# Kernel tuning notes

Hardware: AMD Instinct MI355X
Metric: run time of the kernel (lower is better)

Reference implementation:

```python
import jax, jax.numpy as jnp
import numpy as np
import math

B, N, SEEDS, DIM, H = 16, 2048, 4, 512, 8
DS = DIM // H
EPS = 1e-5
LOG_2PI = math.log(2.0 * math.pi)


def setup_inputs() -> dict:
    key = jax.random.key(0)
    ks = jax.random.split(key, 12)
    s = 1.0 / math.sqrt(DIM)
    d = {}
    d["X"] = jax.random.normal(ks[0], (B, N, SEEDS, DIM), jnp.float32)
    # seed parameters (kaiming/xavier-ish init)
    d["M"] = jax.random.uniform(ks[1], (1, SEEDS, DIM), jnp.float32, -s, s) * math.sqrt(6.0)
    d["S"] = jax.random.uniform(ks[2], (1, SEEDS, DIM), jnp.float32, -s, s) * math.sqrt(6.0)
    d["p"] = jax.random.uniform(ks[3], (1, SEEDS), jnp.float32, -0.5, 0.5)
    # linear layers (PyTorch Linear: y = x @ W.T + b)
    d["Wk"] = jax.random.uniform(ks[4], (DIM, DIM), jnp.float32, -s, s)
    d["bk"] = jax.random.uniform(ks[5], (DIM,), jnp.float32, -s, s)
    d["Wv"] = jax.random.uniform(ks[6], (DIM, DIM), jnp.float32, -s, s)
    d["bv"] = jax.random.uniform(ks[7], (DIM,), jnp.float32, -s, s)
    d["Wo"] = jax.random.uniform(ks[8], (DIM, DIM), jnp.float32, -s, s)
    d["bo"] = jax.random.uniform(ks[9], (DIM,), jnp.float32, -s, s)
    # batchnorm affine params (init: weight=1, bias=0)
    d["g0"] = jnp.ones((SEEDS * DIM,), jnp.float32)
    d["b0"] = jnp.zeros((SEEDS * DIM,), jnp.float32)
    d["g1"] = jnp.ones((SEEDS * DIM,), jnp.float32)
    d["b1"] = jnp.zeros((SEEDS * DIM,), jnp.float32)
    return d


def _batchnorm(x, g, b):
    # BatchNorm1d in training mode: batch stats (biased variance), eps=1e-5
    m = x.mean(axis=0)
    v = x.var(axis=0)
    return g * (x - m) / jnp.sqrt(v + EPS) + b


def reference(X, M, S, p, Wk, bk, Wv, bv, Wo, bo, g0, b0, g1, b1):
    mu = M[0].reshape(SEEDS, H, DS)                      # [S,H,DS] per-head seeds
    sigma = jax.nn.softplus(S[0]).reshape(SEEDS, H, DS)  # [S,H,DS]
    logp = jnp.log(jax.nn.softmax(p[0], axis=-1))        # [S]

    K = (X @ Wk.T + bk).reshape(B, N, SEEDS, H, DS)
    V = (X @ Wv.T + bv).reshape(B, N, SEEDS, H, DS)

    # GMM log-likelihood scores: sum over per-head feature dim
    diff = K - mu                                        # [B,N,S,H,DS]
    ll = (-0.5 * LOG_2PI - jnp.log(sigma) - 0.5 * diff * diff / (sigma * sigma)).sum(-1)
    ll = ll + logp[:, None]                              # [B,N,S,H]

    A = jax.nn.softmax(ll / math.sqrt(DIM), axis=1)      # softmax over instances n
    O = mu + jnp.einsum('bnsh,bnshd->bshd', A, V)        # [B,S,H,DS]
    O = O.reshape(B, SEEDS, DIM)                         # head-major feature concat

    O = _batchnorm(O.reshape(B, SEEDS * DIM), g0, b0).reshape(B, SEEDS, DIM)
    O = O + jax.nn.relu(O @ Wo.T + bo)
    O = _batchnorm(O.reshape(B, SEEDS * DIM), g1, b1).reshape(B, SEEDS, DIM)
    return O
```

## Files before the change

### kernel.cpp

```cpp
#include <hip/hip_runtime.h>
#include <hip/hip_bf16.h>

typedef __attribute__((ext_vector_type(4))) float f32x4;
typedef __attribute__((ext_vector_type(8))) short bf16x8;

constexpr int NB = 16, NN = 2048, NS = 4, NDIM = 512, NH = 8, NDS = 64;
constexpr float LOG2PI = 1.8378770664093453f;
constexpr float INV_SQRT_DIM = 0.04419417382415922f;

__device__ inline short f2bf(float f) {
  __hip_bfloat16 h = __float2bfloat16(f);
  return *reinterpret_cast<short*>(&h);
}
__device__ inline float bf2f(short b) {
  union { unsigned u; float f; } v;
  v.u = ((unsigned)(unsigned short)b) << 16;
  return v.f;
}

__device__ inline void gld16(const void* g, void* l) {
  __builtin_amdgcn_global_load_lds(
      (const __attribute__((address_space(1))) void*)g,
      (__attribute__((address_space(3))) void*)l, 16, 0, 0);
}

__global__ __launch_bounds__(256) void cvtx_kernel(
    const float* __restrict__ in, short* __restrict__ out, int n8)
{
  const int stride = gridDim.x * blockDim.x;
  for (int i = blockIdx.x * blockDim.x + threadIdx.x; i < n8; i += stride) {
    const float4 a = reinterpret_cast<const float4*>(in)[(size_t)i * 2];
    const float4 b = reinterpret_cast<const float4*>(in)[(size_t)i * 2 + 1];
    bf16x8 o;
    o[0] = f2bf(a.x); o[1] = f2bf(a.y); o[2] = f2bf(a.z); o[3] = f2bf(a.w);
    o[4] = f2bf(b.x); o[5] = f2bf(b.y); o[6] = f2bf(b.z); o[7] = f2bf(b.w);
    *reinterpret_cast<bf16x8*>(&out[(size_t)i * 8]) = o;
  }
}

__global__ __launch_bounds__(256) void prep_kernel(
    const float* __restrict__ Wv, float* __restrict__ WvT,
    const float* __restrict__ Wk, short* __restrict__ Wkb,
    const float* __restrict__ Mp, const float* __restrict__ Sp,
    const float* __restrict__ pp, const float* __restrict__ bkp,
    float4* __restrict__ gmm, float* __restrict__ lp2)
{
  const int blk = blockIdx.x;
  const int tid = threadIdx.x;
  if (blk < 1024) {
    const int idx = blk * 256 + tid;
    const int d = idx & 63;
    const int i = (idx >> 6) & 511;
    const int h = idx >> 15;
    WvT[idx] = Wv[(size_t)(h * 64 + d) * 512 + i];
  } else if (blk < 1152) {
    const int j = (blk - 1024) * 256 + tid;
    const float4 a = reinterpret_cast<const float4*>(Wk)[(size_t)j * 2];
    const float4 b = reinterpret_cast<const float4*>(Wk)[(size_t)j * 2 + 1];
    bf16x8 o;
    o[0] = f2bf(a.x); o[1] = f2bf(a.y); o[2] = f2bf(a.z); o[3] = f2bf(a.w);
    o[4] = f2bf(b.x); o[5] = f2bf(b.y); o[6] = f2bf(b.z); o[7] = f2bf(b.w);
    *reinterpret_cast<bf16x8*>(&Wkb[(size_t)j * 8]) = o;
  } else {
    const int idx = (blk - 1152) * 256 + tid;
    const int Jg = idx & 511;
    const float sv = Sp[idx];
    const float sig = log1pf(expf(sv));
    float4 o;
    o.x = Mp[idx];
    o.y = (-0.5f * LOG2PI - logf(sig)) * INV_SQRT_DIM;
    o.z = (0.5f / (sig * sig)) * INV_SQRT_DIM;
    o.w = bkp[Jg];
    gmm[idx] = o;
    if (idx < 4) {
      const float p0 = pp[0], p1 = pp[1], p2 = pp[2], p3 = pp[3];
      const float pmx = fmaxf(fmaxf(p0, p1), fmaxf(p2, p3));
      const float lse = pmx + logf(expf(p0 - pmx) + expf(p1 - pmx) +
                                   expf(p2 - pmx) + expf(p3 - pmx));
      lp2[idx] = (pp[idx] - lse) * INV_SQRT_DIM;
    }
  }
}

__global__ __launch_bounds__(256) void kproj_kernel(
    const short* __restrict__ Xb, const short* __restrict__ Wkb,
    const float4* __restrict__ gmm, const float* __restrict__ lp2,
    float* __restrict__ ll_ws)
{
  __shared__ short As[2][128 * 64];
  __shared__ short Bs[2][128 * 64];

  const int bid0 = blockIdx.x;
  const int bid = (bid0 & 7) * 512 + (bid0 >> 3);
  const int ct = bid & 3;
  const int mt = bid >> 2;
  const int m0 = mt * 128;
  const int c0 = ct * 128;

  const int t = threadIdx.x;
  const int l = t & 63;
  const int w = t >> 6;
  const int wr = w >> 1, wc = w & 1;
  const int lg = l >> 4, lr = l & 15;

  f32x4 acc[4][4] = {};

  const int g8 = (l & 7) ^ (l >> 3);
  const size_t gxa = (size_t)(m0 + w * 32 + (l >> 3)) * NDIM + g8 * 8;
  const size_t gba = (size_t)(c0 + w * 32 + (l >> 3)) * NDIM + g8 * 8;
  const int dA = (w * 32) * 64;

  auto stage = [&](int buf, int ts) {
    const int k0 = ts << 6;
    #pragma unroll
    for (int q = 0; q < 4; ++q) {
      const size_t so = (size_t)(q * 8) * NDIM + k0;
      const int dd = dA + (q * 8) * 64;
      gld16(&Xb[gxa + so],  (char*)&As[buf][dd]);
      gld16(&Wkb[gba + so], (char*)&Bs[buf][dd]);
    }
  };

  auto compute = [&](int buf) {
    #pragma unroll
    for (int kk = 0; kk < 64; kk += 32) {
      bf16x8 a[4], b[4];
      #pragma unroll
      for (int i = 0; i < 4; ++i) {
        const int r = wr * 64 + i * 16 + lr;
        const int byte = r * 128 + ((((kk >> 3) + lg) ^ (lr & 7)) << 4);
        a[i] = *reinterpret_cast<const bf16x8*>((const char*)&As[buf][0] + byte);
      }
      #pragma unroll
      for (int j = 0; j < 4; ++j) {
        const int r = wc * 64 + j * 16 + lr;
        const int byte = r * 128 + ((((kk >> 3) + lg) ^ (lr & 7)) << 4);
        b[j] = *reinterpret_cast<const bf16x8*>((const char*)&Bs[buf][0] + byte);
      }
      #pragma unroll
      for (int i = 0; i < 4; ++i) {
        #pragma unroll
        for (int j = 0; j < 4; ++j)
          acc[i][j] = __builtin_amdgcn_mfma_f32_16x16x32_bf16(a[i], b[j], acc[i][j], 0, 0, 0);
      }
    }
  };

  stage(0, 0);
  __builtin_amdgcn_sched_barrier(0);
  for (int ts = 0; ts < 7; ++ts) {
    stage((ts + 1) & 1, ts + 1);
    asm volatile("s_waitcnt vmcnt(8)" ::: "memory");
    __builtin_amdgcn_s_barrier();
    compute(ts & 1);
    __builtin_amdgcn_s_barrier();
  }
  asm volatile("s_waitcnt vmcnt(0)" ::: "memory");
  __builtin_amdgcn_s_barrier();
  compute(1);
  __builtin_amdgcn_sched_barrier(0);


  const float l0 = lp2[0], l1 = lp2[1], l2 = lp2[2], l3 = lp2[3];
  const float lpv[4] = {l0, l1, l2, l3};

  float part[4][4];
  #pragma unroll
  for (int i = 0; i < 4; ++i)
    #pragma unroll
    for (int e = 0; e < 4; ++e) part[i][e] = 0.f;

  #pragma unroll
  for (int j = 0; j < 4; ++j) {
    const int Jg = c0 + wc * 64 + j * 16 + lr;
    #pragma unroll
    for (int e = 0; e < 4; ++e) {
      const float4 gw = gmm[e * NDIM + Jg];
      #pragma unroll
      for (int i = 0; i < 4; ++i) {
        const float kv = acc[i][j][e] + gw.w;
        const float d = kv - gw.x;
        part[i][e] += gw.y - d * d * gw.z;
      }
    }
  }
  #pragma unroll
  for (int off = 1; off < 16; off <<= 1) {
    #pragma unroll
    for (int i = 0; i < 4; ++i)
      #pragma unroll
      for (int e = 0; e < 4; ++e)
        part[i][e] += __shfl_xor(part[i][e], off, 64);
  }
  if (lr == 0) {
    const int h = ct * 2 + wc;
    #pragma unroll
    for (int i = 0; i < 4; ++i) {
      #pragma unroll
      for (int e = 0; e < 4; ++e) {
        const int R = m0 + wr * 64 + i * 16 + 4 * lg + e;
        const int bn = R >> 2;
        const int bb = bn >> 11;
        const int nn = bn & (NN - 1);
        ll_ws[((size_t)((bb * NS + e) * NH + h)) * NN + nn] = part[i][e] + lpv[e];
      }
    }
  }
}

__global__ __launch_bounds__(256) void stats_kernel(
    const float* __restrict__ ll_ws, float* __restrict__ mxs,
    float* __restrict__ rsum)
{
  __shared__ float sred[8];
  const int g = blockIdx.x;
  const int t = threadIdx.x;
  const int w = t >> 6, l = t & 63;
  const float* ll = ll_ws + (size_t)g * NN;

  float v8[8];
  float mx = -1e30f;
  #pragma unroll
  for (int i = 0; i < 8; ++i) { v8[i] = ll[t + i * 256]; mx = fmaxf(mx, v8[i]); }
  #pragma unroll
  for (int off = 1; off < 64; off <<= 1) mx = fmaxf(mx, __shfl_xor(mx, off, 64));
  if (l == 0) sred[w] = mx;
  __syncthreads();
  mx = fmaxf(fmaxf(sred[0], sred[1]), fmaxf(sred[2], sred[3]));

  float sum = 0.f;
  #pragma unroll
  for (int i = 0; i < 8; ++i) sum += expf(v8[i] - mx);
  #pragma unroll
  for (int off = 1; off < 64; off <<= 1) sum += __shfl_xor(sum, off, 64);
  __syncthreads();
  if (l == 0) sred[4 + w] = sum;
  __syncthreads();
  if (t == 0) {
    mxs[g] = mx;
    rsum[g] = 1.f / (sred[4] + sred[5] + sred[6] + sred[7]);
  }
}

__global__ __launch_bounds__(256) void y_kernel(
    const float* __restrict__ ll_ws, const short* __restrict__ Xb,
    const float* __restrict__ mxs, const float* __restrict__ rsum,
    float* __restrict__ Yp)
{
  __shared__ float wT[256][8];
  const int blk = blockIdx.x;
  const int bs = blk & 63;
  const int nq = blk >> 6;
  const int b = bs >> 2, s = bs & 3;
  const int g0 = bs * 8;
  const int t = threadIdx.x;

  #pragma unroll
  for (int h = 0; h < 8; ++h) {
    const float lv = ll_ws[(size_t)(g0 + h) * NN + nq * 256 + t];
    wT[t][h] = expf(lv - mxs[g0 + h]) * rsum[g0 + h];
  }
  __syncthreads();

  const ushort2* X2 = reinterpret_cast<const ushort2*>(Xb);
  const size_t xbase = ((size_t)(b * 2048 + nq * 256) * 4 + s) * 256 + t;
  float acc[8][2] = {};
  #pragma unroll 4
  for (int n = 0; n < 256; ++n) {
    const ushort2 xv = X2[xbase + (size_t)n * 1024];
    const float x0 = bf2f((short)xv.x), x1 = bf2f((short)xv.y);
    const float4 w0 = *reinterpret_cast<const float4*>(&wT[n][0]);
    const float4 w1 = *reinterpret_cast<const float4*>(&wT[n][4]);
    acc[0][0] += w0.x * x0; acc[0][1] += w0.x * x1;
    acc[1][0] += w0.y * x0; acc[1][1] += w0.y * x1;
    acc[2][0] += w0.z * x0; acc[2][1] += w0.z * x1;
    acc[3][0] += w0.w * x0; acc[3][1] += w0.w * x1;
    acc[4][0] += w1.x * x0; acc[4][1] += w1.x * x1;
    acc[5][0] += w1.y * x0; acc[5][1] += w1.y * x1;
    acc[6][0] += w1.z * x0; acc[6][1] += w1.z * x1;
    acc[7][0] += w1.w * x0; acc[7][1] += w1.w * x1;
  }
  #pragma unroll
  for (int h = 0; h < 8; ++h) {
    float* yp = Yp + ((size_t)((nq * 64 + bs) * 8 + h)) * 512 + 2 * t;
    yp[0] = acc[h][0]; yp[1] = acc[h][1];
  }
}

__global__ __launch_bounds__(256) void poolproj_kernel(
    const float* __restrict__ Yp, const float* __restrict__ WvT,
    const float* __restrict__ bvp, const float* __restrict__ Mp,
    float* __restrict__ O0)
{
  __shared__ float ys[512];
  __shared__ float pr[4][64];
  const int g = blockIdx.x;
  const int bs = g >> 3, h = g & 7;
  const int s = bs & 3;
  const int t = threadIdx.x;

  float a0 = 0.f, a1 = 0.f;
  #pragma unroll
  for (int q = 0; q < 8; ++q) {
    const float* yp = Yp + ((size_t)((q * 64 + bs) * 8 + h)) * 512;
    a0 += yp[t];
    a1 += yp[t + 256];
  }
  ys[t] = a0; ys[t + 256] = a1;
  __syncthreads();

  const int d = t & 63, p = t >> 6;
  const float* wt = WvT + ((size_t)h * 512 + p * 128) * 64 + d;
  const float* yy = ys + p * 128;
  float acc = 0.f;
  #pragma unroll 4
  for (int i = 0; i < 128; ++i) acc += yy[i] * wt[(size_t)i * 64];
  pr[p][d] = acc;
  __syncthreads();
  if (t < 64) {
    const float tot = pr[0][t] + pr[1][t] + pr[2][t] + pr[3][t];
    O0[(size_t)g * 64 + t] = Mp[s * NDIM + h * NDS + t] + bvp[h * 64 + t] + tot;
  }
}

__global__ __launch_bounds__(256) void bn_kernel(
    const float* __restrict__ Xin, const float* __restrict__ gg,
    const float* __restrict__ bb, float* __restrict__ Yo)
{
  const int f = blockIdx.x * 256 + threadIdx.x;
  float x[NB];
  float m = 0.f;
  #pragma unroll
  for (int b = 0; b < NB; ++b) { x[b] = Xin[b * (NS * NDIM) + f]; m += x[b]; }
  m *= (1.f / NB);
  float v = 0.f;
  #pragma unroll
  for (int b = 0; b < NB; ++b) { const float d = x[b] - m; v += d * d; }
  v *= (1.f / NB);
  const float inv = rsqrtf(v + 1e-5f) * gg[f];
  const float bf = bb[f];
  #pragma unroll
  for (int b = 0; b < NB; ++b) Yo[b * (NS * NDIM) + f] = (x[b] - m) * inv + bf;
}

__global__ __launch_bounds__(256) void mlp_kernel(
    const float* __restrict__ Yi, const float* __restrict__ Wo,
    const float* __restrict__ bo, float* __restrict__ Zo)
{
  const int idx = blockIdx.x * 256 + threadIdx.x;
  const int r = idx >> 9, j = idx & 511;
  const float4* yr = reinterpret_cast<const float4*>(Yi + (size_t)r * NDIM);
  const float4* wrow = reinterpret_cast<const float4*>(Wo + (size_t)j * NDIM);
  float acc = 0.f;
  #pragma unroll 4
  for (int i = 0; i < NDIM / 4; ++i) {
    const float4 a = yr[i], b = wrow[i];
    acc += a.x * b.x + a.y * b.y + a.z * b.z + a.w * b.w;
  }
  const float rl = acc + bo[j];
  Zo[idx] = Yi[idx] + fmaxf(rl, 0.f);
}

extern "C" void kernel_launch(void* const* d_in, const int* in_sizes, int n_in,
                              void* d_out, int out_size, void* d_ws, size_t ws_size,
                              hipStream_t stream) {
  (void)in_sizes; (void)n_in; (void)out_size; (void)ws_size;
  const float* X  = (const float*)d_in[0];
  const float* M  = (const float*)d_in[1];
  const float* S  = (const float*)d_in[2];
  const float* p  = (const float*)d_in[3];
  const float* Wk = (const float*)d_in[4];
  const float* bk = (const float*)d_in[5];
  const float* Wv = (const float*)d_in[6];
  const float* bv = (const float*)d_in[7];
  const float* Wo = (const float*)d_in[8];
  const float* bo = (const float*)d_in[9];
  const float* g0 = (const float*)d_in[10];
  const float* b0 = (const float*)d_in[11];
  const float* g1 = (const float*)d_in[12];
  const float* b1 = (const float*)d_in[13];

  char* ws = (char*)d_ws;
  short* Xb    = (short*)ws;
  float* ll_ws = (float*)(ws + (size_t)134217728);
  float* mxs   = (float*)(ws + (size_t)138412032);
  float* rsum  = (float*)(ws + (size_t)138414080);
  float* Yp    = (float*)(ws + (size_t)138416128);
  float* O0    = (float*)(ws + (size_t)146804736);
  float* Y     = (float*)(ws + (size_t)146935808);
  float* Z     = (float*)(ws + (size_t)147066880);
  short* Wkb   = (short*)(ws + (size_t)147197952);
  float* WvT   = (float*)(ws + (size_t)147722240);
  float4* gmm  = (float4*)(ws + (size_t)148770816);
  float* lp2   = (float*)(ws + (size_t)148803584);

  prep_kernel<<<1160, 256, 0, stream>>>(Wv, WvT, Wk, Wkb, M, S, p, bk, gmm, lp2);
  cvtx_kernel<<<2048, 256, 0, stream>>>(X, Xb, 8388608);
  kproj_kernel<<<4096, 256, 0, stream>>>(Xb, Wkb, gmm, lp2, ll_ws);
  stats_kernel<<<512, 256, 0, stream>>>(ll_ws, mxs, rsum);
  y_kernel<<<512, 256, 0, stream>>>(ll_ws, Xb, mxs, rsum, Yp);
  poolproj_kernel<<<512, 256, 0, stream>>>(Yp, WvT, bv, M, O0);
  bn_kernel<<<8, 256, 0, stream>>>(O0, g0, b0, Y);
  mlp_kernel<<<128, 256, 0, stream>>>(Y, Wo, bo, Z);
  bn_kernel<<<8, 256, 0, stream>>>(Z, g1, b1, (float*)d_out);
}
```

Before: 257.7 us.

## Fuse X fp32-to-bf16 conversion into K-projection GEMM A-tile loading

Removes the separate conversion kernel; the K-projection GEMM now loads fp32 X through registers, converts to bf16, writes the swizzled LDS tile, and the ct==0 blocks also store the bf16 copy for the later y_kernel. This eliminates one launch and a full extra pass over X. In exchange each column tile reads fp32 X (twice the bytes), relying on L2 reuse across the four column-tile blocks, and A loads lose the direct global-to-LDS path, adding register pressure.

```diff
diff --git a/kernel.cpp b/kernel.cpp
--- a/kernel.cpp
+++ b/kernel.cpp
@@ -22,20 +22,6 @@
   __builtin_amdgcn_global_load_lds(
       (const __attribute__((address_space(1))) void*)g,
       (__attribute__((address_space(3))) void*)l, 16, 0, 0);
-}
-
-__global__ __launch_bounds__(256) void cvtx_kernel(
-    const float* __restrict__ in, short* __restrict__ out, int n8)
-{
-  const int stride = gridDim.x * blockDim.x;
-  for (int i = blockIdx.x * blockDim.x + threadIdx.x; i < n8; i += stride) {
-    const float4 a = reinterpret_cast<const float4*>(in)[(size_t)i * 2];
-    const float4 b = reinterpret_cast<const float4*>(in)[(size_t)i * 2 + 1];
-    bf16x8 o;
-    o[0] = f2bf(a.x); o[1] = f2bf(a.y); o[2] = f2bf(a.z); o[3] = f2bf(a.w);
-    o[4] = f2bf(b.x); o[5] = f2bf(b.y); o[6] = f2bf(b.z); o[7] = f2bf(b.w);
-    *reinterpret_cast<bf16x8*>(&out[(size_t)i * 8]) = o;
-  }
 }
 
 __global__ __launch_bounds__(256) void prep_kernel(
@@ -83,9 +69,9 @@
 }
 
 __global__ __launch_bounds__(256) void kproj_kernel(
-    const short* __restrict__ Xb, const short* __restrict__ Wkb,
+    const float* __restrict__ X, const short* __restrict__ Wkb,
     const float4* __restrict__ gmm, const float* __restrict__ lp2,
-    float* __restrict__ ll_ws)
+    float* __restrict__ ll_ws, short* __restrict__ Xb)
 {
   __shared__ short As[2][128 * 64];
   __shared__ short Bs[2][128 * 64];
@@ -96,6 +82,7 @@
   const int mt = bid >> 2;
   const int m0 = mt * 128;
   const int c0 = ct * 128;
+  const bool wb = (ct == 0);
 
   const int t = threadIdx.x;
   const int l = t & 63;
@@ -106,18 +93,42 @@
   f32x4 acc[4][4] = {};
 
   const int g8 = (l & 7) ^ (l >> 3);
-  const size_t gxa = (size_t)(m0 + w * 32 + (l >> 3)) * NDIM + g8 * 8;
   const size_t gba = (size_t)(c0 + w * 32 + (l >> 3)) * NDIM + g8 * 8;
-  const int dA = (w * 32) * 64;
-
-  auto stage = [&](int buf, int ts) {
+  const int dB = (w * 32) * 64;
+  auto stageB = [&](int buf, int ts) {
     const int k0 = ts << 6;
     #pragma unroll
-    for (int q = 0; q < 4; ++q) {
-      const size_t so = (size_t)(q * 8) * NDIM + k0;
-      const int dd = dA + (q * 8) * 64;
-      gld16(&Xb[gxa + so],  (char*)&As[buf][dd]);
-      gld16(&Wkb[gba + so], (char*)&Bs[buf][dd]);
+    for (int q = 0; q < 4; ++q)
+      gld16(&Wkb[gba + (size_t)(q * 8) * NDIM + k0], (char*)&Bs[buf][dB + q * 8 * 64]);
+  };
+
+  float4 rA[4][2];
+  auto issueA = [&](int ts) {
+    const int k0 = ts << 6;
+    #pragma unroll
+    for (int u = 0; u < 4; ++u) {
+      const int bc = u * 256 + t;
+      const int row = bc >> 3, c = bc & 7;
+      const float* src = &X[(size_t)(m0 + row) * NDIM + k0 + c * 8];
+      rA[u][0] = *reinterpret_cast<const float4*>(src);
+      rA[u][1] = *reinterpret_cast<const float4*>(src + 4);
+    }
+  };
+  auto cvtWriteA = [&](int buf, int ts) {
+    const int k0 = ts << 6;
+    #pragma unroll
+    for (int u = 0; u < 4; ++u) {
+      const int bc = u * 256 + t;
+      const int row = bc >> 3, c = bc & 7;
+      bf16x8 o;
+      o[0] = f2bf(rA[u][0].x); o[1] = f2bf(rA[u][0].y);
+      o[2] = f2bf(rA[u][0].z); o[3] = f2bf(rA[u][0].w);
+      o[4] = f2bf(rA[u][1].x); o[5] = f2bf(rA[u][1].y);
+      o[6] = f2bf(rA[u][1].z); o[7] = f2bf(rA[u][1].w);
+      *reinterpret_cast<bf16x8*>(
+          (char*)&As[buf][0] + row * 128 + ((c ^ (row & 7)) << 4)) = o;
+      if (wb)
+        *reinterpret_cast<bf16x8*>(&Xb[(size_t)(m0 + row) * NDIM + k0 + c * 8]) = o;
     }
   };
 
@@ -146,11 +157,19 @@
     }
   };
 
-  stage(0, 0);
+  issueA(0);
+  cvtWriteA(0, 0);
+  stageB(0, 0);
+  issueA(1);
+  asm volatile("s_waitcnt vmcnt(8)" ::: "memory");
+  asm volatile("s_waitcnt lgkmcnt(0)" ::: "memory");
+  __builtin_amdgcn_s_barrier();
   __builtin_amdgcn_sched_barrier(0);
   for (int ts = 0; ts < 7; ++ts) {
-    stage((ts + 1) & 1, ts + 1);
-    asm volatile("s_waitcnt vmcnt(8)" ::: "memory");
+    cvtWriteA((ts + 1) & 1, ts + 1);
+    stageB((ts + 1) & 1, ts + 1);
+    if (ts < 6) issueA(ts + 2);
+    asm volatile("s_waitcnt lgkmcnt(0)" ::: "memory");
     __builtin_amdgcn_s_barrier();
     compute(ts & 1);
     __builtin_amdgcn_s_barrier();
@@ -395,8 +414,7 @@
   float* lp2   = (float*)(ws + (size_t)148803584);
 
   prep_kernel<<<1160, 256, 0, stream>>>(Wv, WvT, Wk, Wkb, M, S, p, bk, gmm, lp2);
-  cvtx_kernel<<<2048, 256, 0, stream>>>(X, Xb, 8388608);
-  kproj_kernel<<<4096, 256, 0, stream>>>(Xb, Wkb, gmm, lp2, ll_ws);
+  kproj_kernel<<<4096, 256, 0, stream>>>(X, Wkb, gmm, lp2, ll_ws, Xb);
   stats_kernel<<<512, 256, 0, stream>>>(ll_ws, mxs, rsum);
   y_kernel<<<512, 256, 0, stream>>>(ll_ws, Xb, mxs, rsum, Yp);
   poolproj_kernel<<<512, 256, 0, stream>>>(Yp, WvT, bv, M, O0);
```

Measured after the change: 257.2 us. Within noise of the previous version (-0.2%).

## Fuse softmax stats into pooling via split-softmax and merge small kernels

Applied to the files above, without the earlier changes.

Drops the separate stats kernel. Each y_kernel block now computes a local max and sum over its 256-instance chunk and uses unnormalized exponentials, and poolproj rescales the eight partial results flash-style with a global max and sum. The X conversion is folded into the prep kernel, and the first batchnorm is fused into the MLP kernel, which recomputes the batch statistics redundantly in each block. Together these cut launches and one pass over ll_ws, at the cost of extra reductions inside y_kernel.

```diff
diff --git a/kernel.cpp b/kernel.cpp
--- a/kernel.cpp
+++ b/kernel.cpp
@@ -24,26 +24,13 @@
       (__attribute__((address_space(3))) void*)l, 16, 0, 0);
 }
 
-__global__ __launch_bounds__(256) void cvtx_kernel(
-    const float* __restrict__ in, short* __restrict__ out, int n8)
-{
-  const int stride = gridDim.x * blockDim.x;
-  for (int i = blockIdx.x * blockDim.x + threadIdx.x; i < n8; i += stride) {
-    const float4 a = reinterpret_cast<const float4*>(in)[(size_t)i * 2];
-    const float4 b = reinterpret_cast<const float4*>(in)[(size_t)i * 2 + 1];
-    bf16x8 o;
-    o[0] = f2bf(a.x); o[1] = f2bf(a.y); o[2] = f2bf(a.z); o[3] = f2bf(a.w);
-    o[4] = f2bf(b.x); o[5] = f2bf(b.y); o[6] = f2bf(b.z); o[7] = f2bf(b.w);
-    *reinterpret_cast<bf16x8*>(&out[(size_t)i * 8]) = o;
-  }
-}
-
-__global__ __launch_bounds__(256) void prep_kernel(
+__global__ __launch_bounds__(256) void prepcvt_kernel(
     const float* __restrict__ Wv, float* __restrict__ WvT,
     const float* __restrict__ Wk, short* __restrict__ Wkb,
     const float* __restrict__ Mp, const float* __restrict__ Sp,
     const float* __restrict__ pp, const float* __restrict__ bkp,
-    float4* __restrict__ gmm, float* __restrict__ lp2)
+    float4* __restrict__ gmm, float* __restrict__ lp2,
+    const float* __restrict__ X, short* __restrict__ Xb)
 {
   const int blk = blockIdx.x;
   const int tid = threadIdx.x;
@@ -61,7 +48,7 @@
     o[0] = f2bf(a.x); o[1] = f2bf(a.y); o[2] = f2bf(a.z); o[3] = f2bf(a.w);
     o[4] = f2bf(b.x); o[5] = f2bf(b.y); o[6] = f2bf(b.z); o[7] = f2bf(b.w);
     *reinterpret_cast<bf16x8*>(&Wkb[(size_t)j * 8]) = o;
-  } else {
+  } else if (blk < 1160) {
     const int idx = (blk - 1152) * 256 + tid;
     const int Jg = idx & 511;
     const float sv = Sp[idx];
@@ -79,6 +66,16 @@
                                    expf(p2 - pmx) + expf(p3 - pmx));
       lp2[idx] = (pp[idx] - lse) * INV_SQRT_DIM;
     }
+  } else {
+    const int stride = 2048 * 256;
+    for (int i = (blk - 1160) * 256 + tid; i < 8388608; i += stride) {
+      const float4 a = reinterpret_cast<const float4*>(X)[(size_t)i * 2];
+      const float4 b = reinterpret_cast<const float4*>(X)[(size_t)i * 2 + 1];
+      bf16x8 o;
+      o[0] = f2bf(a.x); o[1] = f2bf(a.y); o[2] = f2bf(a.z); o[3] = f2bf(a.w);
+      o[4] = f2bf(b.x); o[5] = f2bf(b.y); o[6] = f2bf(b.z); o[7] = f2bf(b.w);
+      *reinterpret_cast<bf16x8*>(&Xb[(size_t)i * 8]) = o;
+    }
   }
 }
 
@@ -208,59 +205,47 @@
   }
 }
 
-__global__ __launch_bounds__(256) void stats_kernel(
-    const float* __restrict__ ll_ws, float* __restrict__ mxs,
-    float* __restrict__ rsum)
-{
-  __shared__ float sred[8];
-  const int g = blockIdx.x;
-  const int t = threadIdx.x;
-  const int w = t >> 6, l = t & 63;
-  const float* ll = ll_ws + (size_t)g * NN;
-
-  float v8[8];
-  float mx = -1e30f;
-  #pragma unroll
-  for (int i = 0; i < 8; ++i) { v8[i] = ll[t + i * 256]; mx = fmaxf(mx, v8[i]); }
-  #pragma unroll
-  for (int off = 1; off < 64; off <<= 1) mx = fmaxf(mx, __shfl_xor(mx, off, 64));
-  if (l == 0) sred[w] = mx;
-  __syncthreads();
-  mx = fmaxf(fmaxf(sred[0], sred[1]), fmaxf(sred[2], sred[3]));
-
-  float sum = 0.f;
-  #pragma unroll
-  for (int i = 0; i < 8; ++i) sum += expf(v8[i] - mx);
-  #pragma unroll
-  for (int off = 1; off < 64; off <<= 1) sum += __shfl_xor(sum, off, 64);
-  __syncthreads();
-  if (l == 0) sred[4 + w] = sum;
-  __syncthreads();
-  if (t == 0) {
-    mxs[g] = mx;
-    rsum[g] = 1.f / (sred[4] + sred[5] + sred[6] + sred[7]);
-  }
-}
-
 __global__ __launch_bounds__(256) void y_kernel(
     const float* __restrict__ ll_ws, const short* __restrict__ Xb,
-    const float* __restrict__ mxs, const float* __restrict__ rsum,
-    float* __restrict__ Yp)
+    float* __restrict__ Yp, float2* __restrict__ msws)
 {
   __shared__ float wT[256][8];
+  __shared__ float redm[8][4];
+  __shared__ float reds[8][4];
   const int blk = blockIdx.x;
   const int bs = blk & 63;
   const int nq = blk >> 6;
   const int b = bs >> 2, s = bs & 3;
   const int g0 = bs * 8;
   const int t = threadIdx.x;
-
+  const int w = t >> 6, l = t & 63;
+
+  float lv[8];
   #pragma unroll
   for (int h = 0; h < 8; ++h) {
-    const float lv = ll_ws[(size_t)(g0 + h) * NN + nq * 256 + t];
-    wT[t][h] = expf(lv - mxs[g0 + h]) * rsum[g0 + h];
+    lv[h] = ll_ws[(size_t)(g0 + h) * NN + nq * 256 + t];
+    float mm = lv[h];
+    #pragma unroll
+    for (int off = 1; off < 64; off <<= 1) mm = fmaxf(mm, __shfl_xor(mm, off, 64));
+    if (l == 0) redm[h][w] = mm;
   }
   __syncthreads();
+  float mx[8];
+  #pragma unroll
+  for (int h = 0; h < 8; ++h) {
+    mx[h] = fmaxf(fmaxf(redm[h][0], redm[h][1]), fmaxf(redm[h][2], redm[h][3]));
+    const float e = expf(lv[h] - mx[h]);
+    wT[t][h] = e;
+    float ss = e;
+    #pragma unroll
+    for (int off = 1; off < 64; off <<= 1) ss += __shfl_xor(ss, off, 64);
+    if (l == 0) reds[h][w] = ss;
+  }
+  __syncthreads();
+  if (t < 8) {
+    const float sum = reds[t][0] + reds[t][1] + reds[t][2] + reds[t][3];
+    msws[(size_t)(g0 + t) * 8 + nq] = make_float2(mx[t], sum);
+  }
 
   const ushort2* X2 = reinterpret_cast<const ushort2*>(Xb);
   const size_t xbase = ((size_t)(b * 2048 + nq * 256) * 4 + s) * 256 + t;
@@ -288,9 +273,9 @@
 }
 
 __global__ __launch_bounds__(256) void poolproj_kernel(
-    const float* __restrict__ Yp, const float* __restrict__ WvT,
-    const float* __restrict__ bvp, const float* __restrict__ Mp,
-    float* __restrict__ O0)
+    const float* __restrict__ Yp, const float2* __restrict__ msws,
+    const float* __restrict__ WvT, const float* __restrict__ bvp,
+    const float* __restrict__ Mp, float* __restrict__ O0)
 {
   __shared__ float ys[512];
   __shared__ float pr[4][64];
@@ -299,12 +284,26 @@
   const int s = bs & 3;
   const int t = threadIdx.x;
 
+  const float2* msp = msws + (size_t)g * 8;
+  float M = -1e30f;
+  #pragma unroll
+  for (int q = 0; q < 8; ++q) M = fmaxf(M, msp[q].x);
+  float cq[8];
+  float S = 0.f;
+  #pragma unroll
+  for (int q = 0; q < 8; ++q) {
+    cq[q] = expf(msp[q].x - M);
+    S += msp[q].y * cq[q];
+  }
+  const float rS = 1.f / S;
+
   float a0 = 0.f, a1 = 0.f;
   #pragma unroll
   for (int q = 0; q < 8; ++q) {
     const float* yp = Yp + ((size_t)((q * 64 + bs) * 8 + h)) * 512;
-    a0 += yp[t];
-    a1 += yp[t + 256];
+    const float c = cq[q] * rS;
+    a0 += yp[t] * c;
+    a1 += yp[t + 256] * c;
   }
   ys[t] = a0; ys[t + 256] = a1;
   __syncthreads();
@@ -323,6 +322,47 @@
   }
 }
 
+__global__ __launch_bounds__(256) void bnmlp_kernel(
+    const float* __restrict__ O0, const float* __restrict__ gg,
+    const float* __restrict__ bb, const float* __restrict__ Wo,
+    const float* __restrict__ bo, float* __restrict__ Zo)
+{
+  __shared__ float ys[512];
+  const int blk = blockIdx.x;
+  const int t = threadIdx.x;
+  const int r = blk >> 1;
+  const int b = r >> 2, s = r & 3;
+
+  #pragma unroll
+  for (int u = 0; u < 2; ++u) {
+    const int i = u * 256 + t;
+    const int f = s * 512 + i;
+    float x[NB];
+    float m = 0.f;
+    #pragma unroll
+    for (int bq = 0; bq < NB; ++bq) { x[bq] = O0[bq * 2048 + f]; m += x[bq]; }
+    m *= (1.f / NB);
+    float v = 0.f;
+    #pragma unroll
+    for (int bq = 0; bq < NB; ++bq) { const float d = x[bq] - m; v += d * d; }
+    v *= (1.f / NB);
+    const float inv = rsqrtf(v + 1e-5f) * gg[f];
+    ys[i] = (x[b] - m) * inv + bb[f];
+  }
+  __syncthreads();
+
+  const int j = ((blk & 1) << 8) + t;
+  const float4* yv = reinterpret_cast<const float4*>(ys);
+  const float4* wrow = reinterpret_cast<const float4*>(Wo + (size_t)j * NDIM);
+  float acc = 0.f;
+  #pragma unroll 4
+  for (int i = 0; i < 128; ++i) {
+    const float4 a = yv[i], w = wrow[i];
+    acc += a.x * w.x + a.y * w.y + a.z * w.z + a.w * w.w;
+  }
+  Zo[(size_t)r * 512 + j] = ys[j] + fmaxf(acc + bo[j], 0.f);
+}
+
 __global__ __launch_bounds__(256) void bn_kernel(
     const float* __restrict__ Xin, const float* __restrict__ gg,
     const float* __restrict__ bb, float* __restrict__ Yo)
@@ -341,24 +381,6 @@
   const float bf = bb[f];
   #pragma unroll
   for (int b = 0; b < NB; ++b) Yo[b * (NS * NDIM) + f] = (x[b] - m) * inv + bf;
-}
-
-__global__ __launch_bounds__(256) void mlp_kernel(
-    const float* __restrict__ Yi, const float* __restrict__ Wo,
-    const float* __restrict__ bo, float* __restrict__ Zo)
-{
-  const int idx = blockIdx.x * 256 + threadIdx.x;
-  const int r = idx >> 9, j = idx & 511;
-  const float4* yr = reinterpret_cast<const float4*>(Yi + (size_t)r * NDIM);
-  const float4* wrow = reinterpret_cast<const float4*>(Wo + (size_t)j * NDIM);
-  float acc = 0.f;
-  #pragma unroll 4
-  for (int i = 0; i < NDIM / 4; ++i) {
-    const float4 a = yr[i], b = wrow[i];
-    acc += a.x * b.x + a.y * b.y + a.z * b.z + a.w * b.w;
-  }
-  const float rl = acc + bo[j];
-  Zo[idx] = Yi[idx] + fmaxf(rl, 0.f);
 }
 
 extern "C" void kernel_launch(void* const* d_in, const int* in_sizes, int n_in,
@@ -383,24 +405,20 @@
   char* ws = (char*)d_ws;
   short* Xb    = (short*)ws;
   float* ll_ws = (float*)(ws + (size_t)134217728);
-  float* mxs   = (float*)(ws + (size_t)138412032);
-  float* rsum  = (float*)(ws + (size_t)138414080);
   float* Yp    = (float*)(ws + (size_t)138416128);
   float* O0    = (float*)(ws + (size_t)146804736);
-  float* Y     = (float*)(ws + (size_t)146935808);
   float* Z     = (float*)(ws + (size_t)147066880);
   short* Wkb   = (short*)(ws + (size_t)147197952);
   float* WvT   = (float*)(ws + (size_t)147722240);
   float4* gmm  = (float4*)(ws + (size_t)148770816);
   float* lp2   = (float*)(ws + (size_t)148803584);
-
-  prep_kernel<<<1160, 256, 0, stream>>>(Wv, WvT, Wk, Wkb, M, S, p, bk, gmm, lp2);
-  cvtx_kernel<<<2048, 256, 0, stream>>>(X, Xb, 8388608);
+  float2* msws = (float2*)(ws + (size_t)148803712);
+
+  prepcvt_kernel<<<3208, 256, 0, stream>>>(Wv, WvT, Wk, Wkb, M, S, p, bk,
+                                           gmm, lp2, X, Xb);
   kproj_kernel<<<4096, 256, 0, stream>>>(Xb, Wkb, gmm, lp2, ll_ws);
-  stats_kernel<<<512, 256, 0, stream>>>(ll_ws, mxs, rsum);
-  y_kernel<<<512, 256, 0, stream>>>(ll_ws, Xb, mxs, rsum, Yp);
-  poolproj_kernel<<<512, 256, 0, stream>>>(Yp, WvT, bv, M, O0);
-  bn_kernel<<<8, 256, 0, stream>>>(O0, g0, b0, Y);
-  mlp_kernel<<<128, 256, 0, stream>>>(Y, Wo, bo, Z);
+  y_kernel<<<512, 256, 0, stream>>>(ll_ws, Xb, Yp, msws);
+  poolproj_kernel<<<512, 256, 0, stream>>>(Yp, msws, WvT, bv, M, O0);
+  bnmlp_kernel<<<128, 256, 0, stream>>>(O0, g0, b0, Wo, bo, Z);
   bn_kernel<<<8, 256, 0, stream>>>(Z, g1, b1, (float*)d_out);
 }
```

New measurement: 255.8 us. About the same (-0.8%).
